# Performance work log

Measured on AMD Instinct MI355X. Metric: run time of the kernel, lower is better.

## Reference

```python
import jax, jax.numpy as jnp
import numpy as np

N, E, IN_CH, HID, HEADS, OUT_CH = 100000, 1600000, 512, 8, 8, 16
NEG_SLOPE = 0.2


def setup_inputs() -> dict:
    key = jax.random.key(0)
    ks = jax.random.split(key, 10)
    x = jax.random.normal(ks[0], (N, IN_CH), dtype=jnp.float32)
    edge_index = jax.random.randint(ks[1], (2, E), 0, N, dtype=jnp.int64)
    def glorot(k, shape):
        fan = shape[0] + shape[-1]
        s = jnp.sqrt(6.0 / fan)
        return jax.random.uniform(k, shape, jnp.float32, -s, s)
    W1 = glorot(ks[2], (IN_CH, HEADS * HID))          # conv1 linear
    att_l1 = glorot(ks[3], (HEADS, HID)) * 0.5
    att_r1 = glorot(ks[4], (HEADS, HID)) * 0.5
    b1 = jnp.zeros((HEADS * HID,), jnp.float32)
    W2 = glorot(ks[5], (HEADS * HID, HEADS * OUT_CH))  # conv2 linear
    att_l2 = glorot(ks[6], (HEADS, OUT_CH)) * 0.5
    att_r2 = glorot(ks[7], (HEADS, OUT_CH)) * 0.5
    b2 = jnp.zeros((OUT_CH,), jnp.float32)
    return {"x": x, "edge_index": edge_index, "W1": W1, "att_l1": att_l1,
            "att_r1": att_r1, "b1": b1, "W2": W2, "att_l2": att_l2,
            "att_r2": att_r2, "b2": b2}


def supergat_mx_layer(x, src, dst, W, att_l, att_r, bias, heads, ch, concat):
    n = x.shape[0]
    h = (x @ W).reshape(n, heads, ch)            # [N, H, C]
    x_j = h[src]                                 # [E, H, C] gathered source feats
    x_i = h[dst]                                 # [E, H, C] gathered dest feats
    logits = jnp.sum(x_i * x_j, axis=-1)         # MX dot-product gate [E, H]
    alpha = jnp.sum(x_j * att_l, axis=-1) + jnp.sum(x_i * att_r, axis=-1)
    alpha = alpha * jax.nn.sigmoid(logits)
    alpha = jax.nn.leaky_relu(alpha, NEG_SLOPE)
    # segment softmax over destination neighborhoods
    amax = jax.ops.segment_max(alpha, dst, num_segments=n)
    alpha = jnp.exp(alpha - amax[dst])
    denom = jax.ops.segment_sum(alpha, dst, num_segments=n)
    alpha = alpha / (denom[dst] + 1e-16)
    out = jax.ops.segment_sum(x_j * alpha[..., None], dst, num_segments=n)  # [N, H, C]
    out = out.reshape(n, heads * ch) if concat else out.mean(axis=1)
    return out + bias


def reference(x, edge_index, W1, att_l1, att_r1, b1, W2, att_l2, att_r2, b2):
    n = x.shape[0]
    loop = jnp.arange(n, dtype=edge_index.dtype)
    src = jnp.concatenate([edge_index[0], loop])  # add self loops (PyG default)
    dst = jnp.concatenate([edge_index[1], loop])
    h = supergat_mx_layer(x, src, dst, W1, att_l1, att_r1, b1, HEADS, HID, True)
    h = jax.nn.elu(h)
    out = supergat_mx_layer(h, src, dst, W2, att_l2, att_r2, b2, HEADS, OUT_CH, False)
    return jax.nn.log_softmax(out, axis=-1)
```

## Files before the change

### kernel.cpp

```cpp
#include <hip/hip_runtime.h>
#include <hip/hip_fp16.h>
#include <math.h>

#define N_NODES 100000
#define N_EDGES 1600000
#define EPRIME  (N_EDGES + N_NODES)
#define NEG_SLOPE 0.2f
#define LOG2E 1.44269504f

typedef _Float16 f16x8 __attribute__((ext_vector_type(8)));
typedef float f32x4 __attribute__((ext_vector_type(4)));
typedef float f32x8 __attribute__((ext_vector_type(8)));
typedef float f32x16 __attribute__((ext_vector_type(16)));

__device__ __forceinline__ f32x8 unpack8(float4 r) {
    f32x8 o;
    float2 f;
    f = __half22float2(__builtin_bit_cast(__half2, r.x)); o[0] = f.x; o[1] = f.y;
    f = __half22float2(__builtin_bit_cast(__half2, r.y)); o[2] = f.x; o[3] = f.y;
    f = __half22float2(__builtin_bit_cast(__half2, r.z)); o[4] = f.x; o[5] = f.y;
    f = __half22float2(__builtin_bit_cast(__half2, r.w)); o[6] = f.x; o[7] = f.y;
    return o;
}

__global__ __launch_bounds__(256) void detect_k(const unsigned* __restrict__ w,
                                                unsigned* __restrict__ flag) {
    __shared__ int any;
    if (threadIdx.x == 0) any = 0;
    __syncthreads();
    int nz = 0;
    for (int i = threadIdx.x; i < 1024; i += 256)
        if (w[2 * i + 1] != 0u) nz = 1;
    if (nz) atomicOr(&any, 1);
    __syncthreads();
    if (threadIdx.x == 0) flag[0] = any ? 0u : 1u;
}

__global__ __launch_bounds__(256) void init_k(int* __restrict__ counts,
                                              int* __restrict__ fill) {
    int n = blockIdx.x * blockDim.x + threadIdx.x;
    if (n < N_NODES) { counts[n] = 1; fill[n] = 0; }
}

__global__ __launch_bounds__(256) void count_k(const int* __restrict__ ei,
                                               const unsigned* __restrict__ flag,
                                               int* __restrict__ counts) {
    int e = blockIdx.x * blockDim.x + threadIdx.x;
    if (e >= N_EDGES) return;
    int d = flag[0] ? ei[2 * (N_EDGES + e)] : ei[N_EDGES + e];
    atomicAdd(&counts[d], 1);
}

__global__ __launch_bounds__(256) void scan1_k(const int* __restrict__ counts,
                                               int* __restrict__ rowptr,
                                               int* __restrict__ bsums) {
    __shared__ int s[256];
    int t = threadIdx.x;
    int base = blockIdx.x * 1024 + t * 4;
    int v[4];
#pragma unroll
    for (int j = 0; j < 4; ++j)
        v[j] = (base + j < N_NODES) ? counts[base + j] : 0;
    int tsum = v[0] + v[1] + v[2] + v[3];
    s[t] = tsum;
    __syncthreads();
    for (int off = 1; off < 256; off <<= 1) {
        int x = (t >= off) ? s[t - off] : 0;
        __syncthreads();
        s[t] += x;
        __syncthreads();
    }
    if (t == 255) bsums[blockIdx.x] = s[255];
    int run = s[t] - tsum;
#pragma unroll
    for (int j = 0; j < 4; ++j) {
        if (base + j <= N_NODES) rowptr[base + j] = run;
        run += v[j];
    }
}

__global__ void scan2_k(int* __restrict__ bsums, int nb) {
    if (threadIdx.x == 0 && blockIdx.x == 0) {
        int run = 0;
        for (int i = 0; i < nb; ++i) { int c = bsums[i]; bsums[i] = run; run += c; }
    }
}

__global__ __launch_bounds__(256) void scan3_k(int* __restrict__ rowptr,
                                               const int* __restrict__ bsums) {
    int t = threadIdx.x;
    int base = blockIdx.x * 1024 + t * 4;
    int add = bsums[blockIdx.x];
#pragma unroll
    for (int j = 0; j < 4; ++j)
        if (base + j <= N_NODES) rowptr[base + j] += add;
}

__global__ __launch_bounds__(256) void scatter_k(const int* __restrict__ ei,
                                                 const unsigned* __restrict__ flag,
                                                 const int* __restrict__ rowptr,
                                                 int* __restrict__ fill,
                                                 int* __restrict__ col) {
    int t = blockIdx.x * blockDim.x + threadIdx.x;
    if (t < 8) col[EPRIME + t] = 0;
    if (t >= EPRIME) return;
    int s, d;
    if (t < N_EDGES) {
        if (flag[0]) { s = ei[2 * t]; d = ei[2 * (N_EDGES + t)]; }
        else         { s = ei[t];     d = ei[N_EDGES + t]; }
    } else {
        s = d = t - N_EDGES;
    }
    int pos = rowptr[d] + atomicAdd(&fill[d], 1);
    col[pos] = s;
}

__global__ void hzero_k(int* __restrict__ dbins) {
    if (blockIdx.x == 0) dbins[threadIdx.x] = 0;
}

__global__ __launch_bounds__(256) void hist_k(const int* __restrict__ counts,
                                              int* __restrict__ dbins) {
    __shared__ int lh[256];
    lh[threadIdx.x] = 0;
    __syncthreads();
    int n = blockIdx.x * 256 + threadIdx.x;
    if (n < N_NODES) atomicAdd(&lh[min(counts[n], 255)], 1);
    __syncthreads();
    int c = lh[threadIdx.x];
    if (c) atomicAdd(&dbins[threadIdx.x], c);
}

__global__ __launch_bounds__(256) void hscan_k(const int* __restrict__ dbins,
                                               int* __restrict__ dstart,
                                               int* __restrict__ dfill) {
    __shared__ int s[256];
    int t = threadIdx.x;
    int v = dbins[t];
    s[t] = v;
    __syncthreads();
    for (int off = 1; off < 256; off <<= 1) {
        int x = (t >= off) ? s[t - off] : 0;
        __syncthreads();
        s[t] += x;
        __syncthreads();
    }
    dstart[t] = s[t] - v;
    dfill[t] = 0;
}

__global__ __launch_bounds__(256) void hscatter_k(const int* __restrict__ counts,
                                                  const int* __restrict__ dstart,
                                                  int* __restrict__ dfill,
                                                  int* __restrict__ perm) {
    __shared__ int lh[256];
    __shared__ int lbase[256];
    lh[threadIdx.x] = 0;
    __syncthreads();
    int n = blockIdx.x * 256 + threadIdx.x;
    int b = 0, lrank = 0;
    bool valid = n < N_NODES;
    if (valid) {
        b = min(counts[n], 255);
        lrank = atomicAdd(&lh[b], 1);
    }
    __syncthreads();
    int c = lh[threadIdx.x];
    lbase[threadIdx.x] = c ? atomicAdd(&dfill[threadIdx.x], c) : 0;
    __syncthreads();
    if (valid) perm[dstart[b] + lbase[b] + lrank] = n;
}

__global__ __launch_bounds__(256) void w1cvt_k(const float* __restrict__ W1,
                                               _Float16* __restrict__ W1f) {
    int idx = blockIdx.x * 256 + threadIdx.x;
    if (idx >= 512 * 64) return;
    int j    = idx & 7;
    int lane = (idx >> 3) & 63;
    int nt   = (idx >> 9) & 3;
    int ks   = idx >> 11;
    int k = ks * 32 + (lane >> 4) * 8 + j;
    int c = nt * 16 + (lane & 15);
    W1f[idx] = (_Float16)W1[k * 64 + c];
}

__global__ __launch_bounds__(256) void gemm1_k(const float* __restrict__ x,
                                               const _Float16* __restrict__ W1f,
                                               const float* __restrict__ attl,
                                               const float* __restrict__ attr,
                                               __half* __restrict__ h1,
                                               float* __restrict__ ald,
                                               float* __restrict__ ard) {
    int t = threadIdx.x;
    int w = t >> 6, l = t & 63;
    int rw0 = blockIdx.x * 64 + w * 16;
    int arow = rw0 + (l & 15);
    if (arow >= N_NODES) arow = N_NODES - 1;
    int kg = l >> 4;
    const float4* x4 = (const float4*)(x + (size_t)arow * 512);
    const f16x8* w8 = (const f16x8*)W1f;

    f32x4 acc0 = {0.f, 0.f, 0.f, 0.f};
    f32x4 acc1 = {0.f, 0.f, 0.f, 0.f};
    f32x4 acc2 = {0.f, 0.f, 0.f, 0.f};
    f32x4 acc3 = {0.f, 0.f, 0.f, 0.f};

#pragma unroll 4
    for (int ks = 0; ks < 16; ++ks) {
        float4 a0 = x4[ks * 8 + kg * 2];
        float4 a1 = x4[ks * 8 + kg * 2 + 1];
        f16x8 af;
        af[0] = (_Float16)a0.x; af[1] = (_Float16)a0.y;
        af[2] = (_Float16)a0.z; af[3] = (_Float16)a0.w;
        af[4] = (_Float16)a1.x; af[5] = (_Float16)a1.y;
        af[6] = (_Float16)a1.z; af[7] = (_Float16)a1.w;
        f16x8 b0 = w8[(ks * 4 + 0) * 64 + l];
        f16x8 b1 = w8[(ks * 4 + 1) * 64 + l];
        f16x8 b2 = w8[(ks * 4 + 2) * 64 + l];
        f16x8 b3 = w8[(ks * 4 + 3) * 64 + l];
        acc0 = __builtin_amdgcn_mfma_f32_16x16x32_f16(af, b0, acc0, 0, 0, 0);
        acc1 = __builtin_amdgcn_mfma_f32_16x16x32_f16(af, b1, acc1, 0, 0, 0);
        acc2 = __builtin_amdgcn_mfma_f32_16x16x32_f16(af, b2, acc2, 0, 0, 0);
        acc3 = __builtin_amdgcn_mfma_f32_16x16x32_f16(af, b3, acc3, 0, 0, 0);
    }

    int col = l & 15;
    int hi = col >> 3;
    float al0 = attl[col], al1 = attl[16 + col], al2 = attl[32 + col], al3 = attl[48 + col];
    float ar0 = attr[col], ar1 = attr[16 + col], ar2 = attr[32 + col], ar3 = attr[48 + col];

#pragma unroll
    for (int reg = 0; reg < 4; ++reg) {
        int grow = rw0 + (l >> 4) * 4 + reg;
        bool v = grow < N_NODES;
        float c0 = acc0[reg], c1 = acc1[reg], c2 = acc2[reg], c3 = acc3[reg];
        if (v) {
            __half* hp = h1 + (size_t)grow * 64;
            hp[col]      = __float2half_rn(c0);
            hp[16 + col] = __float2half_rn(c1);
            hp[32 + col] = __float2half_rn(c2);
            hp[48 + col] = __float2half_rn(c3);
        }
        float vl0 = c0 * al0, vl1 = c1 * al1, vl2 = c2 * al2, vl3 = c3 * al3;
        float vr0 = c0 * ar0, vr1 = c1 * ar1, vr2 = c2 * ar2, vr3 = c3 * ar3;
        vl0 += __shfl_xor(vl0, 1); vl1 += __shfl_xor(vl1, 1);
        vl2 += __shfl_xor(vl2, 1); vl3 += __shfl_xor(vl3, 1);
        vr0 += __shfl_xor(vr0, 1); vr1 += __shfl_xor(vr1, 1);
        vr2 += __shfl_xor(vr2, 1); vr3 += __shfl_xor(vr3, 1);
        vl0 += __shfl_xor(vl0, 2); vl1 += __shfl_xor(vl1, 2);
        vl2 += __shfl_xor(vl2, 2); vl3 += __shfl_xor(vl3, 2);
        vr0 += __shfl_xor(vr0, 2); vr1 += __shfl_xor(vr1, 2);
        vr2 += __shfl_xor(vr2, 2); vr3 += __shfl_xor(vr3, 2);
        vl0 += __shfl_xor(vl0, 4); vl1 += __shfl_xor(vl1, 4);
        vl2 += __shfl_xor(vl2, 4); vl3 += __shfl_xor(vl3, 4);
        vr0 += __shfl_xor(vr0, 4); vr1 += __shfl_xor(vr1, 4);
        vr2 += __shfl_xor(vr2, 4); vr3 += __shfl_xor(vr3, 4);
        if (v && (l & 7) == 0) {
            float* alp = ald + (size_t)grow * 8;
            float* arp = ard + (size_t)grow * 8;
            alp[0 + hi] = vl0 * LOG2E; alp[2 + hi] = vl1 * LOG2E;
            alp[4 + hi] = vl2 * LOG2E; alp[6 + hi] = vl3 * LOG2E;
            arp[0 + hi] = vr0 * LOG2E; arp[2 + hi] = vr1 * LOG2E;
            arp[4 + hi] = vr2 * LOG2E; arp[6 + hi] = vr3 * LOG2E;
        }
    }
}

__global__ __launch_bounds__(256) void attn1_k(const __half* __restrict__ h1,
                                               const int* __restrict__ rowptr,
                                               const int* __restrict__ col,
                                               const float* __restrict__ ald,
                                               const float* __restrict__ ard,
                                               const float* __restrict__ b1,
                                               const int* __restrict__ perm,
                                               float* __restrict__ hout) {
    int gid = (blockIdx.x * 256 + threadIdx.x) >> 3;
    int h = threadIdx.x & 7;
    if (gid >= N_NODES) return;
    int node = perm[gid];
    const char* hb = (const char*)h1;
    unsigned hoff = (unsigned)h * 16u;

    f32x8 xi = unpack8(*(const float4*)(hb + (unsigned)node * 128u + hoff));
    float ardi = ard[node * 8 + h];
    int beg = rowptr[node], end = rowptr[node + 1];

    int s0 = col[beg], s1 = col[beg + 1];
    float4 rx0 = *(const float4*)(hb + (unsigned)s0 * 128u + hoff);
    float aj0 = ald[s0 * 8 + h];
    float4 rx1 = *(const float4*)(hb + (unsigned)s1 * 128u + hoff);
    float aj1 = ald[s1 * 8 + h];

    float m2 = -INFINITY, lsum = 0.f;
    f32x8 acc = {0.f, 0.f, 0.f, 0.f, 0.f, 0.f, 0.f, 0.f};
    for (int e = beg; e < end; e += 2) {
        int t0 = col[e + 2], t1 = col[e + 3];
        float4 ry0 = *(const float4*)(hb + (unsigned)t0 * 128u + hoff);
        float c0 = ald[t0 * 8 + h];
        float4 ry1 = *(const float4*)(hb + (unsigned)t1 * 128u + hoff);
        float c1 = ald[t1 * 8 + h];

        f32x8 xj0 = unpack8(rx0);
        f32x8 xj1 = unpack8(rx1);
        float d0 = 0.f, d1 = 0.f;
#pragma unroll
        for (int c = 0; c < 8; ++c) { d0 = fmaf(xi[c], xj0[c], d0); d1 = fmaf(xi[c], xj1[c], d1); }
        float g0 = (aj0 + ardi) * __builtin_amdgcn_rcpf(1.f + __builtin_amdgcn_exp2f(d0 * -LOG2E));
        float g1 = (aj1 + ardi) * __builtin_amdgcn_rcpf(1.f + __builtin_amdgcn_exp2f(d1 * -LOG2E));
        float a0 = fmaxf(g0, NEG_SLOPE * g0);
        float a1 = (e + 1 < end) ? fmaxf(g1, NEG_SLOPE * g1) : -INFINITY;
        float pm = fmaxf(a0, a1);
        if (__any(pm > m2 + 11.5f)) {
            float mn = fmaxf(m2, pm);
            float so = __builtin_amdgcn_exp2f(m2 - mn);
            lsum *= so;
#pragma unroll
            for (int c = 0; c < 8; ++c) acc[c] *= so;
            m2 = mn;
        }
        float p0 = __builtin_amdgcn_exp2f(a0 - m2);
        float p1 = __builtin_amdgcn_exp2f(a1 - m2);
        lsum += p0 + p1;
#pragma unroll
        for (int c = 0; c < 8; ++c) acc[c] += p0 * xj0[c] + p1 * xj1[c];
        rx0 = ry0; aj0 = c0; rx1 = ry1; aj1 = c1;
    }
    float rl = __builtin_amdgcn_rcpf(lsum);
    float4 bv0 = *(const float4*)(b1 + h * 8);
    float4 bv1 = *(const float4*)(b1 + h * 8 + 4);
    float ob[8];
    ob[0] = bv0.x; ob[1] = bv0.y; ob[2] = bv0.z; ob[3] = bv0.w;
    ob[4] = bv1.x; ob[5] = bv1.y; ob[6] = bv1.z; ob[7] = bv1.w;
    float4 o0, o1;
    float* op0 = (float*)&o0;
    float* op1 = (float*)&o1;
#pragma unroll
    for (int c = 0; c < 8; ++c) {
        float o = acc[c] * rl + ob[c];
        o = o > 0.f ? o : (__builtin_amdgcn_exp2f(o * LOG2E) - 1.f);
        if (c < 4) op0[c] = o; else op1[c - 4] = o;
    }
    float4* dst = (float4*)(hout + (size_t)node * 64 + h * 8);
    dst[0] = o0;
    dst[1] = o1;
}

__global__ __launch_bounds__(256) void gemm2_k(const float* __restrict__ h,
                                               const float* __restrict__ W2,
                                               const float* __restrict__ attl,
                                               const float* __restrict__ attr,
                                               __half2* __restrict__ h2,
                                               float* __restrict__ ald,
                                               float* __restrict__ ard) {
    __shared__ float xs[32 * 64];
    int t = threadIdx.x;
    int row0 = blockIdx.x * 32;
    for (int i = t; i < 32 * 16; i += 256) {
        int r = i >> 4, q = i & 15;
        int gr = row0 + r;
        float4 v = make_float4(0.f, 0.f, 0.f, 0.f);
        if (gr < N_NODES) v = ((const float4*)h)[(size_t)gr * 16 + q];
        ((float4*)xs)[r * 16 + q] = v;
    }
    __syncthreads();
    int w = t >> 6, lane = t & 63;
    int r0 = w * 8;
    float2 acc[8];
#pragma unroll
    for (int r = 0; r < 8; ++r) acc[r] = make_float2(0.f, 0.f);
    for (int k = 0; k < 64; ++k) {
        float2 wv = ((const float2*)W2)[k * 64 + lane];
#pragma unroll
        for (int r = 0; r < 8; ++r) {
            float xv = xs[(r0 + r) * 64 + k];
            acc[r].x += xv * wv.x;
            acc[r].y += xv * wv.y;
        }
    }
    float2 al = ((const float2*)attl)[lane];
    float2 ar = ((const float2*)attr)[lane];
#pragma unroll
    for (int r = 0; r < 8; ++r) {
        int gr = row0 + r0 + r;
        float vl = acc[r].x * al.x + acc[r].y * al.y;
        float vr = acc[r].x * ar.x + acc[r].y * ar.y;
        vl += __shfl_xor(vl, 1); vr += __shfl_xor(vr, 1);
        vl += __shfl_xor(vl, 2); vr += __shfl_xor(vr, 2);
        vl += __shfl_xor(vl, 4); vr += __shfl_xor(vr, 4);
        if (gr < N_NODES) {
            h2[(size_t)gr * 64 + lane] = __floats2half2_rn(acc[r].x, acc[r].y);
            if ((lane & 7) == 0) {
                ald[gr * 8 + (lane >> 3)] = vl * LOG2E;
                ard[gr * 8 + (lane >> 3)] = vr * LOG2E;
            }
        }
    }
}

__global__ __launch_bounds__(256) void attn2_k(const __half* __restrict__ h2,
                                               const int* __restrict__ rowptr,
                                               const int* __restrict__ col,
                                               const float* __restrict__ ald,
                                               const float* __restrict__ ard,
                                               const float* __restrict__ b2,
                                               const int* __restrict__ perm,
                                               float* __restrict__ out) {
    int gid = (blockIdx.x * 256 + threadIdx.x) >> 3;
    int h = threadIdx.x & 7;
    if (gid >= N_NODES) return;
    int node = perm[gid];
    const char* hb = (const char*)h2;
    unsigned hoff = (unsigned)h * 32u;

    float4 ri0 = *(const float4*)(hb + (unsigned)node * 256u + hoff);
    float4 ri1 = *(const float4*)(hb + (unsigned)node * 256u + hoff + 16u);
    f32x8 xiA = unpack8(ri0);
    f32x8 xiB = unpack8(ri1);
    float ardi = ard[node * 8 + h];
    int beg = rowptr[node], end = rowptr[node + 1];

    int s0 = col[beg], s1 = col[beg + 1];
    float4 rx0a = *(const float4*)(hb + (unsigned)s0 * 256u + hoff);
    float4 rx0b = *(const float4*)(hb + (unsigned)s0 * 256u + hoff + 16u);
    float aj0 = ald[s0 * 8 + h];
    float4 rx1a = *(const float4*)(hb + (unsigned)s1 * 256u + hoff);
    float4 rx1b = *(const float4*)(hb + (unsigned)s1 * 256u + hoff + 16u);
    float aj1 = ald[s1 * 8 + h];

    float m2 = -INFINITY, lsum = 0.f;
    f32x16 acc;
#pragma unroll
    for (int c = 0; c < 16; ++c) acc[c] = 0.f;

    for (int e = beg; e < end; e += 2) {
        int t0 = col[e + 2], t1 = col[e + 3];
        float4 ry0a = *(const float4*)(hb + (unsigned)t0 * 256u + hoff);
        float4 ry0b = *(const float4*)(hb + (unsigned)t0 * 256u + hoff + 16u);
        float c0 = ald[t0 * 8 + h];
        float4 ry1a = *(const float4*)(hb + (unsigned)t1 * 256u + hoff);
        float4 ry1b = *(const float4*)(hb + (unsigned)t1 * 256u + hoff + 16u);
        float c1 = ald[t1 * 8 + h];

        f32x8 xj0a = unpack8(rx0a), xj0b = unpack8(rx0b);
        f32x8 xj1a = unpack8(rx1a), xj1b = unpack8(rx1b);
        float d0 = 0.f, d1 = 0.f;
#pragma unroll
        for (int c = 0; c < 8; ++c) {
            d0 = fmaf(xiA[c], xj0a[c], d0); d1 = fmaf(xiA[c], xj1a[c], d1);
            d0 = fmaf(xiB[c], xj0b[c], d0); d1 = fmaf(xiB[c], xj1b[c], d1);
        }
        float g0 = (aj0 + ardi) * __builtin_amdgcn_rcpf(1.f + __builtin_amdgcn_exp2f(d0 * -LOG2E));
        float g1 = (aj1 + ardi) * __builtin_amdgcn_rcpf(1.f + __builtin_amdgcn_exp2f(d1 * -LOG2E));
        float a0 = fmaxf(g0, NEG_SLOPE * g0);
        float a1 = (e + 1 < end) ? fmaxf(g1, NEG_SLOPE * g1) : -INFINITY;
        float pm = fmaxf(a0, a1);
        if (__any(pm > m2 + 11.5f)) {
            float mn = fmaxf(m2, pm);
            float so = __builtin_amdgcn_exp2f(m2 - mn);
            lsum *= so;
#pragma unroll
            for (int c = 0; c < 16; ++c) acc[c] *= so;
            m2 = mn;
        }
        float p0 = __builtin_amdgcn_exp2f(a0 - m2);
        float p1 = __builtin_amdgcn_exp2f(a1 - m2);
        lsum += p0 + p1;
#pragma unroll
        for (int c = 0; c < 8; ++c) {
            acc[c]     += p0 * xj0a[c] + p1 * xj1a[c];
            acc[c + 8] += p0 * xj0b[c] + p1 * xj1b[c];
        }
        rx0a = ry0a; rx0b = ry0b; aj0 = c0;
        rx1a = ry1a; rx1b = ry1b; aj1 = c1;
    }

    float rl = __builtin_amdgcn_rcpf(lsum);
    f32x16 v;
#pragma unroll
    for (int c = 0; c < 16; ++c) v[c] = acc[c] * rl;
#pragma unroll
    for (int c = 0; c < 16; ++c) {
        v[c] += __shfl_xor(v[c], 1);
        v[c] += __shfl_xor(v[c], 2);
        v[c] += __shfl_xor(v[c], 4);
    }
    float mx = -INFINITY;
#pragma unroll
    for (int c = 0; c < 16; ++c) { v[c] = v[c] * 0.125f + b2[c]; mx = fmaxf(mx, v[c]); }
    float se = 0.f;
#pragma unroll
    for (int c = 0; c < 16; ++c) se += __expf(v[c] - mx);
    float ls = __logf(se);
    if (h == 0) {
        float4 o;
        float* op = (float*)&o;
        float* dst = out + (size_t)node * 16;
#pragma unroll
        for (int q = 0; q < 4; ++q) {
#pragma unroll
            for (int c = 0; c < 4; ++c) op[c] = v[q * 4 + c] - mx - ls;
            ((float4*)dst)[q] = o;
        }
    }
}

extern "C" void kernel_launch(void* const* d_in, const int* in_sizes, int n_in,
                              void* d_out, int out_size, void* d_ws, size_t ws_size,
                              hipStream_t stream) {
    const float* x     = (const float*)d_in[0];
    const int*   ei    = (const int*)d_in[1];
    const float* W1    = (const float*)d_in[2];
    const float* attl1 = (const float*)d_in[3];
    const float* attr1 = (const float*)d_in[4];
    const float* b1    = (const float*)d_in[5];
    const float* W2    = (const float*)d_in[6];
    const float* attl2 = (const float*)d_in[7];
    const float* attr2 = (const float*)d_in[8];
    const float* b2    = (const float*)d_in[9];
    float* out = (float*)d_out;

    char* ws = (char*)d_ws;
    size_t off = 0;
    auto alloc = [&](size_t bytes) {
        size_t o = off;
        off += (bytes + 255) & ~(size_t)255;
        return o;
    };
    size_t o_flag   = alloc(4);
    size_t o_counts = alloc((size_t)N_NODES * 4);
    size_t o_fill   = alloc((size_t)N_NODES * 4);
    size_t o_rowptr = alloc((size_t)(N_NODES + 1) * 4);
    size_t o_bsums  = alloc(1024 * 4);
    size_t o_col    = alloc((size_t)(EPRIME + 8) * 4);
    size_t o_h1     = alloc((size_t)N_NODES * 64 * 4);
    size_t o_hout   = alloc((size_t)N_NODES * 64 * 4);
    size_t o_h2     = alloc((size_t)N_NODES * 128 * 4);
    size_t o_w1f    = alloc((size_t)512 * 64 * 2);
    size_t o_perm   = alloc((size_t)N_NODES * 4);
    size_t o_dbins  = alloc(256 * 4);
    size_t o_dstart = alloc(256 * 4);
    size_t o_dfill  = alloc(256 * 4);

    size_t aldsz = ((size_t)N_NODES * 8 * 4 + 255) & ~(size_t)255;
    size_t o_ald1 = o_h2;
    size_t o_ard1 = o_h2 + aldsz;
    size_t o_ald2 = o_h1;
    size_t o_ard2 = o_h1 + aldsz;

    unsigned* flag = (unsigned*)(ws + o_flag);
    int* counts = (int*)(ws + o_counts);
    int* fill   = (int*)(ws + o_fill);
    int* rowptr = (int*)(ws + o_rowptr);
    int* bsums  = (int*)(ws + o_bsums);
    int* col    = (int*)(ws + o_col);
    __half* h1  = (__half*)(ws + o_h1);
    float* hout = (float*)(ws + o_hout);
    __half* h2  = (__half*)(ws + o_h2);
    _Float16* w1f = (_Float16*)(ws + o_w1f);
    int* perm   = (int*)(ws + o_perm);
    int* dbins  = (int*)(ws + o_dbins);
    int* dstart = (int*)(ws + o_dstart);
    int* dfill  = (int*)(ws + o_dfill);
    float* ald1 = (float*)(ws + o_ald1);
    float* ard1 = (float*)(ws + o_ard1);
    float* ald2 = (float*)(ws + o_ald2);
    float* ard2 = (float*)(ws + o_ard2);

    int nscan = (N_NODES + 1 + 1023) / 1024;
    int nblk  = (N_NODES + 255) / 256;

    hipLaunchKernelGGL(detect_k, dim3(1), dim3(256), 0, stream, (const unsigned*)ei, flag);
    hipLaunchKernelGGL(init_k, dim3(nblk), dim3(256), 0, stream, counts, fill);
    hipLaunchKernelGGL(count_k, dim3((N_EDGES + 255) / 256), dim3(256), 0, stream, ei, flag, counts);
    hipLaunchKernelGGL(hzero_k, dim3(1), dim3(256), 0, stream, dbins);
    hipLaunchKernelGGL(hist_k, dim3(nblk), dim3(256), 0, stream, counts, dbins);
    hipLaunchKernelGGL(hscan_k, dim3(1), dim3(256), 0, stream, dbins, dstart, dfill);
    hipLaunchKernelGGL(hscatter_k, dim3(nblk), dim3(256), 0, stream, counts, dstart, dfill, perm);
    hipLaunchKernelGGL(scan1_k, dim3(nscan), dim3(256), 0, stream, counts, rowptr, bsums);
    hipLaunchKernelGGL(scan2_k, dim3(1), dim3(64), 0, stream, bsums, nscan);
    hipLaunchKernelGGL(scan3_k, dim3(nscan), dim3(256), 0, stream, rowptr, bsums);
    hipLaunchKernelGGL(scatter_k, dim3((EPRIME + 255) / 256), dim3(256), 0, stream,
                       ei, flag, rowptr, fill, col);
    hipLaunchKernelGGL(w1cvt_k, dim3(128), dim3(256), 0, stream, W1, w1f);
    hipLaunchKernelGGL(gemm1_k, dim3((N_NODES + 63) / 64), dim3(256), 0, stream,
                       x, w1f, attl1, attr1, h1, ald1, ard1);
    hipLaunchKernelGGL(attn1_k, dim3((N_NODES * 8 + 255) / 256), dim3(256), 0, stream,
                       h1, rowptr, col, ald1, ard1, b1, perm, hout);
    hipLaunchKernelGGL(gemm2_k, dim3((N_NODES + 31) / 32), dim3(256), 0, stream,
                       hout, W2, attl2, attr2, (__half2*)h2, ald2, ard2);
    hipLaunchKernelGGL(attn2_k, dim3((N_NODES * 8 + 255) / 256), dim3(256), 0, stream,
                       h2, rowptr, col, ald2, ard2, b2, perm, out);
}
```

Measured before the change: 457.2 us.

## Record edge ranks during counting and scatter CSR without atomics, partitioned by XCD

The counting pass now stores each edge's position within its destination row from the atomicAdd result. That removes the second atomic pass and the fill array from the scatter. Self loops are placed in slot 0 of each row by a separate kernel. The edge scatter is split so each of 8 block groups handles one destination range, aiming for L2-local writes per XCD. The cost is reading edge indices 8 times and a new 6.4MB rank buffer.

```diff
diff --git a/kernel.cpp b/kernel.cpp
--- a/kernel.cpp
+++ b/kernel.cpp
@@ -36,19 +36,19 @@
     if (threadIdx.x == 0) flag[0] = any ? 0u : 1u;
 }
 
-__global__ __launch_bounds__(256) void init_k(int* __restrict__ counts,
-                                              int* __restrict__ fill) {
+__global__ __launch_bounds__(256) void init_k(int* __restrict__ counts) {
     int n = blockIdx.x * blockDim.x + threadIdx.x;
-    if (n < N_NODES) { counts[n] = 1; fill[n] = 0; }
-}
-
-__global__ __launch_bounds__(256) void count_k(const int* __restrict__ ei,
-                                               const unsigned* __restrict__ flag,
-                                               int* __restrict__ counts) {
+    if (n < N_NODES) counts[n] = 1;
+}
+
+__global__ __launch_bounds__(256) void countrank_k(const int* __restrict__ ei,
+                                                   const unsigned* __restrict__ flag,
+                                                   int* __restrict__ counts,
+                                                   int* __restrict__ rank) {
     int e = blockIdx.x * blockDim.x + threadIdx.x;
     if (e >= N_EDGES) return;
     int d = flag[0] ? ei[2 * (N_EDGES + e)] : ei[N_EDGES + e];
-    atomicAdd(&counts[d], 1);
+    rank[e] = atomicAdd(&counts[d], 1);
 }
 
 __global__ __launch_bounds__(256) void scan1_k(const int* __restrict__ counts,
@@ -96,23 +96,31 @@
         if (base + j <= N_NODES) rowptr[base + j] += add;
 }
 
-__global__ __launch_bounds__(256) void scatter_k(const int* __restrict__ ei,
-                                                 const unsigned* __restrict__ flag,
-                                                 const int* __restrict__ rowptr,
-                                                 int* __restrict__ fill,
-                                                 int* __restrict__ col) {
-    int t = blockIdx.x * blockDim.x + threadIdx.x;
-    if (t < 8) col[EPRIME + t] = 0;
-    if (t >= EPRIME) return;
-    int s, d;
-    if (t < N_EDGES) {
-        if (flag[0]) { s = ei[2 * t]; d = ei[2 * (N_EDGES + t)]; }
-        else         { s = ei[t];     d = ei[N_EDGES + t]; }
-    } else {
-        s = d = t - N_EDGES;
-    }
-    int pos = rowptr[d] + atomicAdd(&fill[d], 1);
-    col[pos] = s;
+__global__ __launch_bounds__(256) void selfloop_k(const int* __restrict__ rowptr,
+                                                  int* __restrict__ col) {
+    int n = blockIdx.x * blockDim.x + threadIdx.x;
+    if (n < 8) col[EPRIME + n] = 0;
+    if (n < N_NODES) col[rowptr[n]] = n;
+}
+
+#define SCHUNK 2048
+__global__ __launch_bounds__(256) void scatter2_k(const int* __restrict__ ei,
+                                                  const unsigned* __restrict__ flag,
+                                                  const int* __restrict__ rowptr,
+                                                  const int* __restrict__ rank,
+                                                  int* __restrict__ col) {
+    int xcd = blockIdx.x & 7;
+    int base = (blockIdx.x >> 3) * SCHUNK;
+    int lo = xcd * 12500, hi = lo + 12500;
+    int lim = min(base + SCHUNK, N_EDGES);
+    bool f = flag[0] != 0;
+    for (int i = base + threadIdx.x; i < lim; i += 256) {
+        int d = f ? ei[2 * (N_EDGES + i)] : ei[N_EDGES + i];
+        if (d >= lo && d < hi) {
+            int s = f ? ei[2 * i] : ei[i];
+            col[rowptr[d] + rank[i]] = s;
+        }
+    }
 }
 
 __global__ void hzero_k(int* __restrict__ dbins) {
@@ -528,7 +536,7 @@
     };
     size_t o_flag   = alloc(4);
     size_t o_counts = alloc((size_t)N_NODES * 4);
-    size_t o_fill   = alloc((size_t)N_NODES * 4);
+    size_t o_rank   = alloc((size_t)N_EDGES * 4);
     size_t o_rowptr = alloc((size_t)(N_NODES + 1) * 4);
     size_t o_bsums  = alloc(1024 * 4);
     size_t o_col    = alloc((size_t)(EPRIME + 8) * 4);
@@ -549,7 +557,7 @@
 
     unsigned* flag = (unsigned*)(ws + o_flag);
     int* counts = (int*)(ws + o_counts);
-    int* fill   = (int*)(ws + o_fill);
+    int* rank   = (int*)(ws + o_rank);
     int* rowptr = (int*)(ws + o_rowptr);
     int* bsums  = (int*)(ws + o_bsums);
     int* col    = (int*)(ws + o_col);
@@ -568,10 +576,12 @@
 
     int nscan = (N_NODES + 1 + 1023) / 1024;
     int nblk  = (N_NODES + 255) / 256;
+    int nscat = 8 * ((N_EDGES + SCHUNK - 1) / SCHUNK);
 
     hipLaunchKernelGGL(detect_k, dim3(1), dim3(256), 0, stream, (const unsigned*)ei, flag);
-    hipLaunchKernelGGL(init_k, dim3(nblk), dim3(256), 0, stream, counts, fill);
-    hipLaunchKernelGGL(count_k, dim3((N_EDGES + 255) / 256), dim3(256), 0, stream, ei, flag, counts);
+    hipLaunchKernelGGL(init_k, dim3(nblk), dim3(256), 0, stream, counts);
+    hipLaunchKernelGGL(countrank_k, dim3((N_EDGES + 255) / 256), dim3(256), 0, stream,
+                       ei, flag, counts, rank);
     hipLaunchKernelGGL(hzero_k, dim3(1), dim3(256), 0, stream, dbins);
     hipLaunchKernelGGL(hist_k, dim3(nblk), dim3(256), 0, stream, counts, dbins);
     hipLaunchKernelGGL(hscan_k, dim3(1), dim3(256), 0, stream, dbins, dstart, dfill);
@@ -579,8 +589,9 @@
     hipLaunchKernelGGL(scan1_k, dim3(nscan), dim3(256), 0, stream, counts, rowptr, bsums);
     hipLaunchKernelGGL(scan2_k, dim3(1), dim3(64), 0, stream, bsums, nscan);
     hipLaunchKernelGGL(scan3_k, dim3(nscan), dim3(256), 0, stream, rowptr, bsums);
-    hipLaunchKernelGGL(scatter_k, dim3((EPRIME + 255) / 256), dim3(256), 0, stream,
-                       ei, flag, rowptr, fill, col);
+    hipLaunchKernelGGL(selfloop_k, dim3(nblk), dim3(256), 0, stream, rowptr, col);
+    hipLaunchKernelGGL(scatter2_k, dim3(nscat), dim3(256), 0, stream,
+                       ei, flag, rowptr, rank, col);
     hipLaunchKernelGGL(w1cvt_k, dim3(128), dim3(256), 0, stream, W1, w1f);
     hipLaunchKernelGGL(gemm1_k, dim3((N_NODES + 63) / 64), dim3(256), 0, stream,
                        x, w1f, attl1, attr1, h1, ald1, ard1);
```

Measured after the change: 406.8 us. 11.0% less time.
